# Performance work log

Measured on AMD Instinct MI355X. Metric: run time of the kernel, lower is better.

The kernel has to match this reference:

```python
import jax, jax.numpy as jnp
import numpy as np

N_QUBITS = 10
DEPTH = 2
RZ_ANGLE = 0.1
BATCH = 8192
INPUT_DIM = 128

# --- precomputed constants over the 2^n basis ---
def _z_axis(i):
    shape = [1] * N_QUBITS
    shape[i] = 2
    return np.array([1.0, -1.0], np.float32).reshape(shape)

_Z_NP = [np.broadcast_to(_z_axis(i), (2,) * N_QUBITS) for i in range(N_QUBITS)]
_ZSUM = np.zeros((2,) * N_QUBITS, np.float32)
for _z in _Z_NP:
    _ZSUM = _ZSUM + _z
# RZ(phi) = diag(e^{-i phi/2}, e^{+i phi/2}); applying it to every qubit once
# multiplies each basis state by exp(-i*(phi/2)*sum_i z_i)
_RZ_PHASE = jnp.asarray(np.exp(-1j * (RZ_ANGLE / 2.0) * _ZSUM).astype(np.complex64))
_Z = [jnp.asarray(z) for z in _Z_NP]


def _apply_1q(state, gate, wire):
    # state: [2]*n complex, gate: [2,2] complex
    state = jnp.moveaxis(state, wire, 0)
    shape = state.shape
    state = gate @ state.reshape(2, -1)
    return jnp.moveaxis(state.reshape(shape), 0, wire)


def _apply_cnot(state, ctrl, tgt):
    state = jnp.moveaxis(state, (ctrl, tgt), (0, 1))
    shape = state.shape
    s = state.reshape(2, 2, -1)
    s = jnp.stack([s[0], s[1, ::-1]], axis=0)  # flip target where control==1
    return jnp.moveaxis(s.reshape(shape), (0, 1), (ctrl, tgt))


def _circuit(theta):
    # theta: [n_qubits] rotation angles -> [n_qubits] Pauli-Z expectations
    state = jnp.zeros((2,) * N_QUBITS, jnp.complex64).at[(0,) * N_QUBITS].set(1.0)
    for i in range(N_QUBITS):
        half = theta[i] * 0.5
        c = jnp.cos(half).astype(jnp.complex64)
        s = jnp.sin(half).astype(jnp.complex64)
        g = jnp.stack([jnp.stack([c, -1j * s]), jnp.stack([-1j * s, c])])  # RX(theta)
        state = _apply_1q(state, g, i)
    for _ in range(DEPTH):
        state = state * _RZ_PHASE  # RZ(0.1) on every wire, fused
        for i in range(N_QUBITS - 1):
            state = _apply_cnot(state, i, i + 1)
    probs = state.real ** 2 + state.imag ** 2
    return jnp.stack([jnp.sum(probs * z) for z in _Z])


_qgate = jax.vmap(_circuit)  # [B, n_qubits] -> [B, n_qubits]


def setup_inputs() -> dict:
    key = jax.random.key(0)
    ks = jax.random.split(key, 12)
    d = INPUT_DIM + N_QUBITS
    w = lambda k: jax.random.normal(k, (N_QUBITS, d), jnp.float32) * 0.1
    b = lambda k: jax.random.normal(k, (N_QUBITS,), jnp.float32) * 0.1
    return {
        "x": jax.random.normal(ks[0], (BATCH, INPUT_DIM), jnp.float32),
        "hx": jax.random.normal(ks[1], (BATCH, N_QUBITS), jnp.float32),
        "cx": jax.random.normal(ks[2], (BATCH, N_QUBITS), jnp.float32),
        "Wf": w(ks[3]), "bf": b(ks[4]),
        "Wi": w(ks[5]), "bi": b(ks[6]),
        "Wu": w(ks[7]), "bu": b(ks[8]),
        "Wo": w(ks[9]), "bo": b(ks[10]),
    }


def reference(x, hx, cx, Wf, bf, Wi, bi, Wu, bu, Wo, bo):
    comb = jnp.concatenate([x, hx], axis=1)  # [B, input_dim+hidden]
    f = jax.nn.sigmoid(_qgate(comb @ Wf.T + bf))
    i = jax.nn.sigmoid(_qgate(comb @ Wi.T + bi))
    g = jnp.tanh(_qgate(comb @ Wu.T + bu))
    o = jax.nn.sigmoid(_qgate(comb @ Wo.T + bo))
    c_new = f * cx + i * g
    h_new = o * jnp.tanh(c_new)
    return (h_new, c_new)
```

## Files before the change

kernel.cpp:

```cpp
#include <hip/hip_runtime.h>

#define BATCH_N 8192
#define NQ 10
#define CD 138
#define CPAD 140
#define RT 32
#define NJ 40

__global__ __launch_bounds__(256) void qlstm_kernel(
    const float* __restrict__ x,  const float* __restrict__ hx, const float* __restrict__ cx,
    const float* __restrict__ Wf, const float* __restrict__ bf,
    const float* __restrict__ Wi, const float* __restrict__ bi,
    const float* __restrict__ Wu, const float* __restrict__ bu,
    const float* __restrict__ Wo, const float* __restrict__ bo,
    float* __restrict__ out)
{
    __shared__ float sW[NJ][CPAD];
    __shared__ float sComb[RT][CPAD];
    __shared__ float sB[NJ];
    __shared__ float sTheta[RT][44];
    __shared__ float sGate[4][RT][NQ];

    const int tid = threadIdx.x;
    const int r0  = blockIdx.x * RT;

    const float* Ws[4] = {Wf, Wi, Wu, Wo};
    const float* bs[4] = {bf, bi, bu, bo};

    #pragma unroll
    for (int g = 0; g < 4; ++g) {
        for (int idx = tid; idx < NQ * CD; idx += 256) {
            int j = idx / CD;
            int k = idx - j * CD;
            sW[g * NQ + j][k] = Ws[g][idx];
        }
    }
    if (tid < 2 * NJ) sW[tid >> 1][CD + (tid & 1)] = 0.f;
    if (tid < NJ)     sB[tid] = bs[tid / NQ][tid % NQ];

    {
        const float4* x4 = (const float4*)(x + (size_t)r0 * 128);
        for (int idx = tid; idx < RT * 32; idx += 256) {
            int row = idx >> 5;
            int c4  = idx & 31;
            float4 v = x4[idx];
            *(float4*)&sComb[row][c4 * 4] = v;
        }
    }
    for (int idx = tid; idx < RT * NQ; idx += 256) {
        int row = idx / NQ;
        int q   = idx - row * NQ;
        sComb[row][128 + q] = hx[(size_t)r0 * NQ + idx];
    }
    if (tid < 2 * RT) sComb[tid >> 1][CD + (tid & 1)] = 0.f;

    __syncthreads();

    {
        const int r  = tid & 31;
        const int j0 = (tid >> 5) * 5;
        float acc[5];
        #pragma unroll
        for (int jj = 0; jj < 5; ++jj) acc[jj] = sB[j0 + jj];
        for (int k4 = 0; k4 < CPAD / 4; ++k4) {
            float4 xv = *(const float4*)&sComb[r][k4 * 4];
            #pragma unroll
            for (int jj = 0; jj < 5; ++jj) {
                float4 wv = *(const float4*)&sW[j0 + jj][k4 * 4];
                acc[jj] = fmaf(xv.x, wv.x, acc[jj]);
                acc[jj] = fmaf(xv.y, wv.y, acc[jj]);
                acc[jj] = fmaf(xv.z, wv.z, acc[jj]);
                acc[jj] = fmaf(xv.w, wv.w, acc[jj]);
            }
        }
        #pragma unroll
        for (int jj = 0; jj < 5; ++jj) sTheta[r][j0 + jj] = acc[jj];
    }
    __syncthreads();

    if (tid < 4 * RT) {
        const int r = tid & 31;
        const int g = tid >> 5;
        float z[NQ];
        #pragma unroll
        for (int q = 0; q < NQ; ++q) {
            float c = cosf(sTheta[r][g * NQ + q]);
            z[q] = (q < 2) ? c : z[q - 2] * c;
        }
        #pragma unroll
        for (int q = 0; q < NQ; ++q) {
            float zz = z[q];
            float val = (g == 2) ? tanhf(zz) : 1.f / (1.f + expf(-zz));
            sGate[g][r][q] = val;
        }
    }
    __syncthreads();

    const float* fG = &sGate[0][0][0];
    const float* iG = &sGate[1][0][0];
    const float* gG = &sGate[2][0][0];
    const float* oG = &sGate[3][0][0];
    for (int idx = tid; idx < RT * NQ; idx += 256) {
        float fv  = fG[idx];
        float iv  = iG[idx];
        float gv  = gG[idx];
        float ov  = oG[idx];
        float cxv = cx[(size_t)r0 * NQ + idx];
        float cn  = fv * cxv + iv * gv;
        float hn  = ov * tanhf(cn);
        out[(size_t)r0 * NQ + idx] = hn;
        out[(size_t)BATCH_N * NQ + (size_t)r0 * NQ + idx] = cn;
    }
}

extern "C" void kernel_launch(void* const* d_in, const int* in_sizes, int n_in,
                              void* d_out, int out_size, void* d_ws, size_t ws_size,
                              hipStream_t stream) {
    const float* x  = (const float*)d_in[0];
    const float* hx = (const float*)d_in[1];
    const float* cx = (const float*)d_in[2];
    const float* Wf = (const float*)d_in[3];
    const float* bf = (const float*)d_in[4];
    const float* Wi = (const float*)d_in[5];
    const float* bi = (const float*)d_in[6];
    const float* Wu = (const float*)d_in[7];
    const float* bu = (const float*)d_in[8];
    const float* Wo = (const float*)d_in[9];
    const float* bo = (const float*)d_in[10];
    float* out = (float*)d_out;

    dim3 grid(BATCH_N / RT);
    dim3 block(256);
    hipLaunchKernelGGL(qlstm_kernel, grid, block, 0, stream,
                       x, hx, cx, Wf, bf, Wi, bi, Wu, bu, Wo, bo, out);
}
```

Measured before the change: 16.89 us.

## Read gate weights via wave-uniform scalar loads and fuse projection with gate evaluation

Drops the LDS staging of all four weight matrices. Each wavefront is now assigned one gate and reads that gate's weights straight from global memory with wave-uniform addresses, which can become scalar loads. Each lane computes all 10 angles for one row and evaluates the cos-product and activation in registers, so the theta LDS buffer and one barrier go away. cx loads are prefetched at kernel start. The cost is that only half the lanes in each wave do the projection, which concentrates that work.

```diff
diff --git a/kernel.cpp b/kernel.cpp
--- a/kernel.cpp
+++ b/kernel.cpp
@@ -5,7 +5,6 @@
 #define CD 138
 #define CPAD 140
 #define RT 32
-#define NJ 40
 
 __global__ __launch_bounds__(256) void qlstm_kernel(
     const float* __restrict__ x,  const float* __restrict__ hx, const float* __restrict__ cx,
@@ -15,101 +14,94 @@
     const float* __restrict__ Wo, const float* __restrict__ bo,
     float* __restrict__ out)
 {
-    __shared__ float sW[NJ][CPAD];
     __shared__ float sComb[RT][CPAD];
-    __shared__ float sB[NJ];
-    __shared__ float sTheta[RT][44];
     __shared__ float sGate[4][RT][NQ];
 
     const int tid = threadIdx.x;
     const int r0  = blockIdx.x * RT;
 
-    const float* Ws[4] = {Wf, Wi, Wu, Wo};
-    const float* bs[4] = {bf, bi, bu, bo};
-
-    #pragma unroll
-    for (int g = 0; g < 4; ++g) {
-        for (int idx = tid; idx < NQ * CD; idx += 256) {
-            int j = idx / CD;
-            int k = idx - j * CD;
-            sW[g * NQ + j][k] = Ws[g][idx];
-        }
-    }
-    if (tid < 2 * NJ) sW[tid >> 1][CD + (tid & 1)] = 0.f;
-    if (tid < NJ)     sB[tid] = bs[tid / NQ][tid % NQ];
+    float cx0 = cx[(size_t)r0 * NQ + tid];
+    float cx1 = (tid < RT * NQ - 256)
+              ? cx[(size_t)r0 * NQ + 256 + tid] : 0.f;
 
     {
         const float4* x4 = (const float4*)(x + (size_t)r0 * 128);
-        for (int idx = tid; idx < RT * 32; idx += 256) {
-            int row = idx >> 5;
-            int c4  = idx & 31;
+        #pragma unroll
+        for (int it = 0; it < 4; ++it) {
+            int idx = tid + it * 256;
             float4 v = x4[idx];
-            *(float4*)&sComb[row][c4 * 4] = v;
+            *(float4*)&sComb[idx >> 5][(idx & 31) * 4] = v;
         }
     }
-    for (int idx = tid; idx < RT * NQ; idx += 256) {
-        int row = idx / NQ;
-        int q   = idx - row * NQ;
-        sComb[row][128 + q] = hx[(size_t)r0 * NQ + idx];
+    if (tid < 160) {
+        float2 h2 = ((const float2*)(hx + (size_t)r0 * NQ))[tid];
+        int f = tid * 2;
+        int row = f / NQ;
+        int q   = f - row * NQ;
+        sComb[row][128 + q]     = h2.x;
+        sComb[row][128 + q + 1] = h2.y;
     }
     if (tid < 2 * RT) sComb[tid >> 1][CD + (tid & 1)] = 0.f;
 
     __syncthreads();
 
     {
-        const int r  = tid & 31;
-        const int j0 = (tid >> 5) * 5;
-        float acc[5];
-        #pragma unroll
-        for (int jj = 0; jj < 5; ++jj) acc[jj] = sB[j0 + jj];
-        for (int k4 = 0; k4 < CPAD / 4; ++k4) {
-            float4 xv = *(const float4*)&sComb[r][k4 * 4];
+        const int w    = __builtin_amdgcn_readfirstlane(tid >> 6);
+        const int lane = tid & 63;
+        const float* Wg = (w == 0) ? Wf : (w == 1) ? Wi : (w == 2) ? Wu : Wo;
+        const float* Bg = (w == 0) ? bf : (w == 1) ? bi : (w == 2) ? bu : bo;
+
+        if (lane < RT) {
+            const int r = lane;
+            float acc[NQ];
             #pragma unroll
-            for (int jj = 0; jj < 5; ++jj) {
-                float4 wv = *(const float4*)&sW[j0 + jj][k4 * 4];
-                acc[jj] = fmaf(xv.x, wv.x, acc[jj]);
-                acc[jj] = fmaf(xv.y, wv.y, acc[jj]);
-                acc[jj] = fmaf(xv.z, wv.z, acc[jj]);
-                acc[jj] = fmaf(xv.w, wv.w, acc[jj]);
+            for (int q = 0; q < NQ; ++q) acc[q] = Bg[q];
+
+            for (int k4 = 0; k4 < CPAD / 4; ++k4) {
+                float4 xv = *(const float4*)&sComb[r][k4 * 4];
+                #pragma unroll
+                for (int q = 0; q < NQ; ++q) {
+                    const float* wp = Wg + q * CD + k4 * 4;
+                    float2 wa = *(const float2*)(wp);
+                    float2 wb = *(const float2*)(wp + 2);
+                    acc[q] = fmaf(xv.x, wa.x, acc[q]);
+                    acc[q] = fmaf(xv.y, wa.y, acc[q]);
+                    acc[q] = fmaf(xv.z, wb.x, acc[q]);
+                    acc[q] = fmaf(xv.w, wb.y, acc[q]);
+                }
             }
-        }
-        #pragma unroll
-        for (int jj = 0; jj < 5; ++jj) sTheta[r][j0 + jj] = acc[jj];
-    }
-    __syncthreads();
 
-    if (tid < 4 * RT) {
-        const int r = tid & 31;
-        const int g = tid >> 5;
-        float z[NQ];
-        #pragma unroll
-        for (int q = 0; q < NQ; ++q) {
-            float c = cosf(sTheta[r][g * NQ + q]);
-            z[q] = (q < 2) ? c : z[q - 2] * c;
-        }
-        #pragma unroll
-        for (int q = 0; q < NQ; ++q) {
-            float zz = z[q];
-            float val = (g == 2) ? tanhf(zz) : 1.f / (1.f + expf(-zz));
-            sGate[g][r][q] = val;
+            float z[NQ];
+            #pragma unroll
+            for (int q = 0; q < NQ; ++q) {
+                float c = cosf(acc[q]);
+                z[q] = (q < 2) ? c : z[q - 2] * c;
+            }
+            #pragma unroll
+            for (int q = 0; q < NQ; ++q) {
+                float zz = z[q];
+                float val = (w == 2) ? tanhf(zz) : 1.f / (1.f + expf(-zz));
+                sGate[w][r][q] = val;
+            }
         }
     }
     __syncthreads();
 
-    const float* fG = &sGate[0][0][0];
-    const float* iG = &sGate[1][0][0];
-    const float* gG = &sGate[2][0][0];
-    const float* oG = &sGate[3][0][0];
-    for (int idx = tid; idx < RT * NQ; idx += 256) {
-        float fv  = fG[idx];
-        float iv  = iG[idx];
-        float gv  = gG[idx];
-        float ov  = oG[idx];
-        float cxv = cx[(size_t)r0 * NQ + idx];
-        float cn  = fv * cxv + iv * gv;
-        float hn  = ov * tanhf(cn);
-        out[(size_t)r0 * NQ + idx] = hn;
-        out[(size_t)BATCH_N * NQ + (size_t)r0 * NQ + idx] = cn;
+    const float* G = &sGate[0][0][0];
+    #pragma unroll
+    for (int it = 0; it < 2; ++it) {
+        int idx = tid + it * 256;
+        if (idx < RT * NQ) {
+            float cxv = it ? cx1 : cx0;
+            float fv = G[idx];
+            float iv = G[idx + RT * NQ];
+            float gv = G[idx + 2 * RT * NQ];
+            float ov = G[idx + 3 * RT * NQ];
+            float cn = fv * cxv + iv * gv;
+            float hn = ov * tanhf(cn);
+            out[(size_t)r0 * NQ + idx] = hn;
+            out[(size_t)BATCH_N * NQ + (size_t)r0 * NQ + idx] = cn;
+        }
     }
 }
 
```

Measured after the change: 18.42 us. 9.0% more time.
